# Kernel tuning notes

Measured on AMD Instinct MI355X. Metric: run time of the kernel, lower is better.

Reference implementation:

```python
import jax, jax.numpy as jnp
import numpy as np


def _segsum(x):
    """Stable segment sum: exp(segsum(A)) is 1-semiseparable. x: (..., T) -> (..., T, T)."""
    T = x.shape[-1]
    xx = jnp.broadcast_to(x[..., None], (*x.shape, T))
    xx = jnp.where(jnp.tril(jnp.ones((T, T), bool), -1), xx, 0.0)
    s = jnp.cumsum(xx, axis=-2)
    return jnp.where(jnp.tril(jnp.ones((T, T), bool), 0), s, -jnp.inf)


def setup_inputs() -> dict:
    key = jax.random.key(0)
    ks = jax.random.split(key, 6)
    b, T, h, p, n = 2, 1024, 32, 64, 128
    x = jax.random.normal(ks[0], (b, T, h, p), jnp.float32)
    # negative decay rates, as produced by -exp(A_log)*softplus(dt) in Mamba2
    A = -jax.random.uniform(ks[1], (b, T, h), jnp.float32, minval=0.01, maxval=0.5)
    B = jax.random.normal(ks[2], (b, T, h, n), jnp.float32)
    C = jax.random.normal(ks[3], (b, T, h, n), jnp.float32)
    # retrieval similarity mask (lower-triangular, like segment_and_cosine_similarity output)
    L_mask = jax.random.uniform(ks[4], (b, h, T, T), jnp.float32) * jnp.tril(jnp.ones((T, T), jnp.float32))
    mask_scaling_factor = jnp.float32(0.5)
    return {"x": x, "A": A, "B": B, "C": C, "L_mask": L_mask,
            "mask_scaling_factor": mask_scaling_factor, "chunk_size": 64}


def reference(x, A, B, C, L_mask, mask_scaling_factor, chunk_size):
    b, T, h, p = x.shape
    n = B.shape[-1]
    l = chunk_size
    k = T // l
    # chunk: b (c l) ... -> b c l ...
    xr = x.reshape(b, k, l, h, p)
    Br = B.reshape(b, k, l, h, n)
    Cr = C.reshape(b, k, l, h, n)
    Ar = jnp.transpose(A.reshape(b, k, l, h), (0, 3, 1, 2))  # b h c l
    A_cs = jnp.cumsum(Ar, axis=-1)                            # b h c l
    L = jnp.exp(_segsum(Ar))                                  # b h c l l
    # decompose_diagonal_and_lower_tri(L_mask, chunk_size)
    r = L_mask.reshape(b, h, k, l, k, l)
    didx = np.arange(k)
    L_mask_diag = jnp.moveaxis(r[:, :, didx, :, didx, :], 0, 2)          # b h k l l
    row_idx, col_idx = np.tril_indices(k, -1)                             # strict lower block pairs
    lower_tri = jnp.moveaxis(r[:, :, row_idx, :, col_idx, :], 0, 2)       # b h P l l
    L = L + mask_scaling_factor * L_mask_diag
    # diagonal (intra-chunk) blocks
    Y_diag = jnp.einsum('bclhn,bcshn,bhcls,bcshp->bclhp', Cr, Br, L, xr)
    # retrieval off-diagonal blocks, scatter-added back per destination chunk
    Y_tmp = jnp.einsum('bclhn,bcshn,bhcls,bcshp->bclhp',
                       Cr[:, row_idx], Br[:, col_idx],
                       mask_scaling_factor * lower_tri, xr[:, col_idx])   # b P l h p
    Y_retr = jnp.moveaxis(
        jax.ops.segment_sum(jnp.moveaxis(Y_tmp, 1, 0), jnp.asarray(row_idx), num_segments=k),
        0, 1)                                                             # b k l h p
    # inter-chunk state passing
    decay_states = jnp.exp(A_cs[..., -1:] - A_cs)                         # b h c l
    states = jnp.einsum('bclhn,bhcl,bclhp->bchpn', Br, decay_states, xr)  # b c h p n
    states = jnp.concatenate([jnp.zeros_like(states[:, :1]), states], axis=1)
    decay_chunk = jnp.exp(_segsum(jnp.pad(A_cs[..., -1], ((0, 0), (0, 0), (1, 0)))))  # b h (k+1) (k+1)
    new_states = jnp.einsum('bhzc,bchpn->bzhpn', decay_chunk, states)
    states_in, final_state = new_states[:, :-1], new_states[:, -1]
    Y_off = jnp.einsum('bclhn,bchpn,bhcl->bclhp', Cr, states_in, jnp.exp(A_cs))
    Y = (Y_diag + Y_off + Y_retr).reshape(b, T, h, p)
    return Y, final_state
```

## Files before the change

### kernel.cpp

```cpp
#include <hip/hip_runtime.h>

#define T_ 1024
#define H_ 32
#define P_ 64
#define N_ 128
#define L_ 64

typedef float f32x4 __attribute__((ext_vector_type(4)));
typedef short short8 __attribute__((ext_vector_type(8)));
typedef short short4v __attribute__((ext_vector_type(4)));

static __device__ __forceinline__ unsigned short f2bf(float f) {
  unsigned int u = __float_as_uint(f);
  u = u + 0x7fffu + ((u >> 16) & 1u);
  return (unsigned short)(u >> 16);
}

__global__ __launch_bounds__(1024) void cuma_kernel(const float* __restrict__ A,
                                                    float* __restrict__ cumA) {
  const int bh = blockIdx.x;
  const int b = bh >> 5, h = bh & 31;
  const int t = threadIdx.x;
  __shared__ float s[1024];
  s[t] = A[(b * T_ + t) * H_ + h];
  __syncthreads();
  for (int off = 1; off < 1024; off <<= 1) {
    float v = (t >= off) ? s[t - off] : 0.0f;
    __syncthreads();
    s[t] += v;
    __syncthreads();
  }
  cumA[bh * T_ + t] = s[t];
}

__global__ __launch_bounds__(256, 3) void attn_kernel(
    const float* __restrict__ x, const float* __restrict__ Bm,
    const float* __restrict__ Cm, const float* __restrict__ mask,
    const float* __restrict__ msf_p, const float* __restrict__ cumA,
    float* __restrict__ Y) {
  const int qc = 15 - (int)blockIdx.x;
  const int bh = blockIdx.y;
  const int b = bh >> 5, h = bh & 31;
  const float msf = msf_p[0];

  __shared__ short Cs[64][136];
  __shared__ short Bs[64][136];
  __shared__ short Xt[64][72];
  __shared__ short Ps[64][72];
  __shared__ float cAq[64];
  __shared__ float cAk[64];

  const int tid = threadIdx.x;
  const int wv = tid >> 6;
  const int lane = tid & 63;
  const int q = lane >> 4;
  const int c = lane & 15;

  {
    const float* Cg = Cm + ((size_t)(b * T_ + qc * L_) * H_ + h) * N_;
#pragma unroll
    for (int it = 0; it < 8; ++it) {
      const int idx = tid + 256 * it;
      const int row = idx >> 5, k4 = idx & 31;
      const float4 v = *(const float4*)(Cg + (size_t)row * (H_ * N_) + k4 * 4);
      short4v o;
      o.x = (short)f2bf(v.x); o.y = (short)f2bf(v.y);
      o.z = (short)f2bf(v.z); o.w = (short)f2bf(v.w);
      *(short4v*)&Cs[row][k4 * 4] = o;
    }
    if (tid < 64) cAq[tid] = cumA[bh * T_ + qc * L_ + tid];
  }

  f32x4 yacc[4];
#pragma unroll
  for (int pt = 0; pt < 4; ++pt) yacc[pt] = (f32x4){0.f, 0.f, 0.f, 0.f};

  for (int kc = 0; kc <= qc; ++kc) {
    float m_pre[16];
    {
      const float* mbase = mask + ((size_t)bh * T_ + (size_t)(qc * L_ + 16 * wv + 4 * q)) * T_ +
                           (size_t)kc * L_ + c;
#pragma unroll
      for (int tj = 0; tj < 4; ++tj)
#pragma unroll
        for (int r = 0; r < 4; ++r)
          m_pre[tj * 4 + r] = mbase[(size_t)r * T_ + 16 * tj];
    }

    __syncthreads();

    {
      const float* Bg = Bm + ((size_t)(b * T_ + kc * L_) * H_ + h) * N_;
#pragma unroll
      for (int it = 0; it < 8; ++it) {
        const int idx = tid + 256 * it;
        const int row = idx >> 5, k4 = idx & 31;
        const float4 v = *(const float4*)(Bg + (size_t)row * (H_ * N_) + k4 * 4);
        short4v o;
        o.x = (short)f2bf(v.x); o.y = (short)f2bf(v.y);
        o.z = (short)f2bf(v.z); o.w = (short)f2bf(v.w);
        *(short4v*)&Bs[row][k4 * 4] = o;
      }
      const float* xg = x + ((size_t)(b * T_ + kc * L_) * H_ + h) * P_;
#pragma unroll
      for (int it = 0; it < 4; ++it) {
        const int idx = tid + 256 * it;
        const int j = idx >> 4, p4 = idx & 15;
        const float4 v = *(const float4*)(xg + (size_t)j * (H_ * P_) + p4 * 4);
        Xt[p4 * 4 + 0][j] = (short)f2bf(v.x);
        Xt[p4 * 4 + 1][j] = (short)f2bf(v.y);
        Xt[p4 * 4 + 2][j] = (short)f2bf(v.z);
        Xt[p4 * 4 + 3][j] = (short)f2bf(v.w);
      }
      if (tid < 64) cAk[tid] = cumA[bh * T_ + kc * L_ + tid];
    }
    __syncthreads();

    f32x4 sacc[4];
#pragma unroll
    for (int tj = 0; tj < 4; ++tj) sacc[tj] = (f32x4){0.f, 0.f, 0.f, 0.f};
#pragma unroll
    for (int kt = 0; kt < 4; ++kt) {
      const int k0 = kt * 32;
      const short8 af = *(const short8*)&Cs[16 * wv + c][k0 + 8 * q];
#pragma unroll
      for (int tj = 0; tj < 4; ++tj) {
        const short8 bf = *(const short8*)&Bs[16 * tj + c][k0 + 8 * q];
        sacc[tj] = __builtin_amdgcn_mfma_f32_16x16x32_bf16(af, bf, sacc[tj], 0, 0, 0);
      }
    }

    float ca_i[4], ck_j[4];
#pragma unroll
    for (int r = 0; r < 4; ++r) ca_i[r] = cAq[16 * wv + 4 * q + r];
#pragma unroll
    for (int tj = 0; tj < 4; ++tj) ck_j[tj] = cAk[16 * tj + c];
    const bool diag = (kc == qc);
#pragma unroll
    for (int tj = 0; tj < 4; ++tj) {
      const int j_l = 16 * tj + c;
#pragma unroll
      for (int r = 0; r < 4; ++r) {
        const int i_l = 16 * wv + 4 * q + r;
        float wgt = __expf(ca_i[r] - ck_j[tj]) + msf * m_pre[tj * 4 + r];
        if (diag && j_l > i_l) wgt = 0.0f;
        Ps[i_l][j_l] = (short)f2bf(sacc[tj][r] * wgt);
      }
    }
    __syncthreads();

#pragma unroll
    for (int kt = 0; kt < 2; ++kt) {
      const int k0 = kt * 32;
      const short8 pf = *(const short8*)&Ps[16 * wv + c][k0 + 8 * q];
#pragma unroll
      for (int pt = 0; pt < 4; ++pt) {
        const short8 xf = *(const short8*)&Xt[16 * pt + c][k0 + 8 * q];
        yacc[pt] = __builtin_amdgcn_mfma_f32_16x16x32_bf16(pf, xf, yacc[pt], 0, 0, 0);
      }
    }
  }

  float* Yg = Y + ((size_t)(b * T_ + qc * L_) * H_ + h) * P_;
#pragma unroll
  for (int pt = 0; pt < 4; ++pt)
#pragma unroll
    for (int r = 0; r < 4; ++r)
      Yg[(size_t)(16 * wv + 4 * q + r) * (H_ * P_) + 16 * pt + c] = yacc[pt][r];
}

__global__ __launch_bounds__(512) void state_kernel(
    const float* __restrict__ x, const float* __restrict__ Bm,
    const float* __restrict__ cumA, float* __restrict__ out) {
  const int bh = blockIdx.x;
  const int pg = blockIdx.y;
  const int b = bh >> 5, h = bh & 31;
  const int tid = threadIdx.x;
  const int n = tid & 127;
  const int th = tid >> 7;
  const int pbase = pg * 8;

  __shared__ float wsh[1024];
  __shared__ float red[3][8][128];
  {
    const float cend = cumA[bh * T_ + (T_ - 1)];
    for (int t = tid; t < 1024; t += 512)
      wsh[t] = __expf(cend - cumA[bh * T_ + t]);
  }
  __syncthreads();

  float acc[8];
#pragma unroll
  for (int pp = 0; pp < 8; ++pp) acc[pp] = 0.0f;

  const int t0 = th * 256;
#pragma unroll 4
  for (int it = 0; it < 256; ++it) {
    const int t = t0 + it;
    const float bv = Bm[((size_t)(b * T_ + t) * H_ + h) * N_ + n] * wsh[t];
    const float* xp = x + ((size_t)(b * T_ + t) * H_ + h) * P_ + pbase;
#pragma unroll
    for (int pp = 0; pp < 8; ++pp) acc[pp] += bv * xp[pp];
  }

  if (th > 0) {
#pragma unroll
    for (int pp = 0; pp < 8; ++pp) red[th - 1][pp][n] = acc[pp];
  }
  __syncthreads();
  if (th == 0) {
    float* o = out + (size_t)bh * P_ * N_;
#pragma unroll
    for (int pp = 0; pp < 8; ++pp) {
      const float s = acc[pp] + red[0][pp][n] + red[1][pp][n] + red[2][pp][n];
      o[(size_t)(pbase + pp) * N_ + n] = s;
    }
  }
}

extern "C" void kernel_launch(void* const* d_in, const int* in_sizes, int n_in,
                              void* d_out, int out_size, void* d_ws, size_t ws_size,
                              hipStream_t stream) {
  const float* x    = (const float*)d_in[0];
  const float* A    = (const float*)d_in[1];
  const float* Bm   = (const float*)d_in[2];
  const float* Cm   = (const float*)d_in[3];
  const float* mask = (const float*)d_in[4];
  const float* msf  = (const float*)d_in[5];
  float* Y  = (float*)d_out;
  float* fs = (float*)d_out + (size_t)2 * T_ * H_ * P_;
  float* cumA = (float*)d_ws;

  cuma_kernel<<<64, 1024, 0, stream>>>(A, cumA);
  attn_kernel<<<dim3(16, 64), 256, 0, stream>>>(x, Bm, Cm, mask, msf, cumA, Y);
  state_kernel<<<dim3(64, 8), 512, 0, stream>>>(x, Bm, cumA, fs);
}
```

Before: 539.6 us.

## Pre-convert B and x to bf16 layouts and use MFMA for final state

Adds prep kernels that convert B and x to bf16 once, including transposed copies, stored in workspace. The attention kernel then reads those operands straight from global memory into MFMA fragments with no shared-memory staging or block barriers, keeps C fragments in registers, and orders blocks so that all heads of one query chunk are launched together. The state kernel is rewritten to use bf16 MFMA over the transposed tensors instead of scalar FP32 FMAs. This removes the repeated per-block conversion of B and x, but adds extra launches and workspace traffic, and the final state now uses bf16 rounding of the decay-weighted x.

Result: no change. 539.0 us (-0.1%).

```diff
diff --git a/kernel.cpp b/kernel.cpp
--- a/kernel.cpp
+++ b/kernel.cpp
@@ -12,8 +12,11 @@
 
 static __device__ __forceinline__ unsigned short f2bf(float f) {
   unsigned int u = __float_as_uint(f);
-  u = u + 0x7fffu + ((u >> 16) & 1u);
+  u += 0x7fffu + ((u >> 16) & 1u);
   return (unsigned short)(u >> 16);
+}
+static __device__ __forceinline__ float bf2f(short s) {
+  return __uint_as_float(((unsigned int)(unsigned short)s) << 16);
 }
 
 __global__ __launch_bounds__(1024) void cuma_kernel(const float* __restrict__ A,
@@ -33,155 +36,185 @@
   cumA[bh * T_ + t] = s[t];
 }
 
-__global__ __launch_bounds__(256, 3) void attn_kernel(
-    const float* __restrict__ x, const float* __restrict__ Bm,
+__global__ __launch_bounds__(256) void prep_b(const float* __restrict__ Bm,
+                                              short* __restrict__ Bbf,
+                                              short* __restrict__ BT) {
+  const int bh = blockIdx.x;
+  const int tb = blockIdx.y;
+  const int b = bh >> 5, h = bh & 31;
+  const int tid = threadIdx.x;
+  __shared__ short Bt[128][72];
+#pragma unroll
+  for (int i = 0; i < 8; ++i) {
+    const int idx = tid + 256 * i;
+    const int row = idx >> 5, n4 = idx & 31;
+    const float4 v = *(const float4*)(Bm + ((size_t)(b * T_ + tb * 64 + row) * H_ + h) * N_ + n4 * 4);
+    short4v o;
+    o.x = (short)f2bf(v.x); o.y = (short)f2bf(v.y);
+    o.z = (short)f2bf(v.z); o.w = (short)f2bf(v.w);
+    *(short4v*)(Bbf + ((size_t)bh * T_ + tb * 64 + row) * N_ + n4 * 4) = o;
+    Bt[n4 * 4 + 0][row] = o.x; Bt[n4 * 4 + 1][row] = o.y;
+    Bt[n4 * 4 + 2][row] = o.z; Bt[n4 * 4 + 3][row] = o.w;
+  }
+  __syncthreads();
+#pragma unroll
+  for (int i = 0; i < 4; ++i) {
+    const int idx = tid + 256 * i;
+    const int n = idx >> 3, t8 = idx & 7;
+    const short4v a = *(const short4v*)&Bt[n][t8 * 8];
+    const short4v c = *(const short4v*)&Bt[n][t8 * 8 + 4];
+    short8 o;
+    o[0] = a.x; o[1] = a.y; o[2] = a.z; o[3] = a.w;
+    o[4] = c.x; o[5] = c.y; o[6] = c.z; o[7] = c.w;
+    *(short8*)(BT + ((size_t)bh * N_ + n) * T_ + tb * 64 + t8 * 8) = o;
+  }
+}
+
+__global__ __launch_bounds__(256) void prep_x(const float* __restrict__ x,
+                                              short* __restrict__ xT) {
+  const int bh = blockIdx.x, tb = blockIdx.y;
+  const int b = bh >> 5, h = bh & 31;
+  const int tid = threadIdx.x;
+  __shared__ short Xt[64][72];
+#pragma unroll
+  for (int i = 0; i < 4; ++i) {
+    const int idx = tid + 256 * i;
+    const int row = idx >> 4, p4 = idx & 15;
+    const float4 v = *(const float4*)(x + ((size_t)(b * T_ + tb * 64 + row) * H_ + h) * P_ + p4 * 4);
+    Xt[p4 * 4 + 0][row] = (short)f2bf(v.x);
+    Xt[p4 * 4 + 1][row] = (short)f2bf(v.y);
+    Xt[p4 * 4 + 2][row] = (short)f2bf(v.z);
+    Xt[p4 * 4 + 3][row] = (short)f2bf(v.w);
+  }
+  __syncthreads();
+#pragma unroll
+  for (int i = 0; i < 2; ++i) {
+    const int idx = tid + 256 * i;
+    const int p = idx >> 3, t8 = idx & 7;
+    const short4v a = *(const short4v*)&Xt[p][t8 * 8];
+    const short4v c = *(const short4v*)&Xt[p][t8 * 8 + 4];
+    short8 o;
+    o[0] = a.x; o[1] = a.y; o[2] = a.z; o[3] = a.w;
+    o[4] = c.x; o[5] = c.y; o[6] = c.z; o[7] = c.w;
+    *(short8*)(xT + ((size_t)bh * P_ + p) * T_ + tb * 64 + t8 * 8) = o;
+  }
+}
+
+__global__ __launch_bounds__(256, 4) void attn_kernel(
+    const short* __restrict__ xT, const short* __restrict__ Bbf,
     const float* __restrict__ Cm, const float* __restrict__ mask,
     const float* __restrict__ msf_p, const float* __restrict__ cumA,
     float* __restrict__ Y) {
-  const int qc = 15 - (int)blockIdx.x;
-  const int bh = blockIdx.y;
+  const int blk = blockIdx.x;
+  const int qc = 15 - (blk >> 6);
+  const int bh = blk & 63;
   const int b = bh >> 5, h = bh & 31;
   const float msf = msf_p[0];
-
-  __shared__ short Cs[64][136];
-  __shared__ short Bs[64][136];
-  __shared__ short Xt[64][72];
-  __shared__ short Ps[64][72];
-  __shared__ float cAq[64];
-  __shared__ float cAk[64];
-
-  const int tid = threadIdx.x;
-  const int wv = tid >> 6;
+  const int tid = threadIdx.x;
+  const int w = tid >> 6;
   const int lane = tid & 63;
-  const int q = lane >> 4;
-  const int c = lane & 15;
-
+  const int q = lane >> 4, c = lane & 15;
+
+  __shared__ short Ps[4][16][72];
+
+  short8 cf[4];
   {
-    const float* Cg = Cm + ((size_t)(b * T_ + qc * L_) * H_ + h) * N_;
-#pragma unroll
-    for (int it = 0; it < 8; ++it) {
-      const int idx = tid + 256 * it;
-      const int row = idx >> 5, k4 = idx & 31;
-      const float4 v = *(const float4*)(Cg + (size_t)row * (H_ * N_) + k4 * 4);
-      short4v o;
-      o.x = (short)f2bf(v.x); o.y = (short)f2bf(v.y);
-      o.z = (short)f2bf(v.z); o.w = (short)f2bf(v.w);
-      *(short4v*)&Cs[row][k4 * 4] = o;
-    }
-    if (tid < 64) cAq[tid] = cumA[bh * T_ + qc * L_ + tid];
-  }
+    const float* Cg = Cm + ((size_t)(b * T_ + qc * L_ + 16 * w + c) * H_ + h) * N_ + 8 * q;
+#pragma unroll
+    for (int kt = 0; kt < 4; ++kt) {
+      const float4 v0 = *(const float4*)(Cg + kt * 32);
+      const float4 v1 = *(const float4*)(Cg + kt * 32 + 4);
+      short8 f;
+      f[0] = (short)f2bf(v0.x); f[1] = (short)f2bf(v0.y);
+      f[2] = (short)f2bf(v0.z); f[3] = (short)f2bf(v0.w);
+      f[4] = (short)f2bf(v1.x); f[5] = (short)f2bf(v1.y);
+      f[6] = (short)f2bf(v1.z); f[7] = (short)f2bf(v1.w);
+      cf[kt] = f;
+    }
+  }
+  float ca_i[4];
+#pragma unroll
+  for (int r = 0; r < 4; ++r)
+    ca_i[r] = cumA[bh * T_ + qc * L_ + 16 * w + 4 * q + r];
 
   f32x4 yacc[4];
 #pragma unroll
   for (int pt = 0; pt < 4; ++pt) yacc[pt] = (f32x4){0.f, 0.f, 0.f, 0.f};
 
   for (int kc = 0; kc <= qc; ++kc) {
-    float m_pre[16];
+    float mv[16];
     {
-      const float* mbase = mask + ((size_t)bh * T_ + (size_t)(qc * L_ + 16 * wv + 4 * q)) * T_ +
+      const float* mbase = mask + ((size_t)bh * T_ + (size_t)(qc * L_ + 16 * w + 4 * q)) * T_ +
                            (size_t)kc * L_ + c;
 #pragma unroll
       for (int tj = 0; tj < 4; ++tj)
 #pragma unroll
         for (int r = 0; r < 4; ++r)
-          m_pre[tj * 4 + r] = mbase[(size_t)r * T_ + 16 * tj];
-    }
-
-    __syncthreads();
-
-    {
-      const float* Bg = Bm + ((size_t)(b * T_ + kc * L_) * H_ + h) * N_;
-#pragma unroll
-      for (int it = 0; it < 8; ++it) {
-        const int idx = tid + 256 * it;
-        const int row = idx >> 5, k4 = idx & 31;
-        const float4 v = *(const float4*)(Bg + (size_t)row * (H_ * N_) + k4 * 4);
-        short4v o;
-        o.x = (short)f2bf(v.x); o.y = (short)f2bf(v.y);
-        o.z = (short)f2bf(v.z); o.w = (short)f2bf(v.w);
-        *(short4v*)&Bs[row][k4 * 4] = o;
+          mv[tj * 4 + r] = mbase[(size_t)r * T_ + 16 * tj];
+    }
+    float ck[4];
+#pragma unroll
+    for (int tj = 0; tj < 4; ++tj)
+      ck[tj] = cumA[bh * T_ + kc * L_ + 16 * tj + c];
+
+    f32x4 sacc[4];
+#pragma unroll
+    for (int tj = 0; tj < 4; ++tj) sacc[tj] = (f32x4){0.f, 0.f, 0.f, 0.f};
+    const short* Bg = Bbf + ((size_t)bh * T_ + kc * L_) * N_ + 8 * q;
+#pragma unroll
+    for (int kt = 0; kt < 4; ++kt) {
+#pragma unroll
+      for (int tj = 0; tj < 4; ++tj) {
+        const short8 bf = *(const short8*)(Bg + (size_t)(16 * tj + c) * N_ + kt * 32);
+        sacc[tj] = __builtin_amdgcn_mfma_f32_16x16x32_bf16(cf[kt], bf, sacc[tj], 0, 0, 0);
       }
-      const float* xg = x + ((size_t)(b * T_ + kc * L_) * H_ + h) * P_;
-#pragma unroll
-      for (int it = 0; it < 4; ++it) {
-        const int idx = tid + 256 * it;
-        const int j = idx >> 4, p4 = idx & 15;
-        const float4 v = *(const float4*)(xg + (size_t)j * (H_ * P_) + p4 * 4);
-        Xt[p4 * 4 + 0][j] = (short)f2bf(v.x);
-        Xt[p4 * 4 + 1][j] = (short)f2bf(v.y);
-        Xt[p4 * 4 + 2][j] = (short)f2bf(v.z);
-        Xt[p4 * 4 + 3][j] = (short)f2bf(v.w);
-      }
-      if (tid < 64) cAk[tid] = cumA[bh * T_ + kc * L_ + tid];
-    }
-    __syncthreads();
-
-    f32x4 sacc[4];
-#pragma unroll
-    for (int tj = 0; tj < 4; ++tj) sacc[tj] = (f32x4){0.f, 0.f, 0.f, 0.f};
-#pragma unroll
-    for (int kt = 0; kt < 4; ++kt) {
-      const int k0 = kt * 32;
-      const short8 af = *(const short8*)&Cs[16 * wv + c][k0 + 8 * q];
-#pragma unroll
-      for (int tj = 0; tj < 4; ++tj) {
-        const short8 bf = *(const short8*)&Bs[16 * tj + c][k0 + 8 * q];
-        sacc[tj] = __builtin_amdgcn_mfma_f32_16x16x32_bf16(af, bf, sacc[tj], 0, 0, 0);
-      }
-    }
-
-    float ca_i[4], ck_j[4];
-#pragma unroll
-    for (int r = 0; r < 4; ++r) ca_i[r] = cAq[16 * wv + 4 * q + r];
-#pragma unroll
-    for (int tj = 0; tj < 4; ++tj) ck_j[tj] = cAk[16 * tj + c];
+    }
+
     const bool diag = (kc == qc);
 #pragma unroll
     for (int tj = 0; tj < 4; ++tj) {
       const int j_l = 16 * tj + c;
 #pragma unroll
       for (int r = 0; r < 4; ++r) {
-        const int i_l = 16 * wv + 4 * q + r;
-        float wgt = __expf(ca_i[r] - ck_j[tj]) + msf * m_pre[tj * 4 + r];
+        const int i_l = 16 * w + 4 * q + r;
+        float wgt = __expf(ca_i[r] - ck[tj]) + msf * mv[tj * 4 + r];
         if (diag && j_l > i_l) wgt = 0.0f;
-        Ps[i_l][j_l] = (short)f2bf(sacc[tj][r] * wgt);
+        Ps[w][4 * q + r][j_l] = (short)f2bf(sacc[tj][r] * wgt);
       }
     }
-    __syncthreads();
-
-#pragma unroll
-    for (int kt = 0; kt < 2; ++kt) {
-      const int k0 = kt * 32;
-      const short8 pf = *(const short8*)&Ps[16 * wv + c][k0 + 8 * q];
+
+#pragma unroll
+    for (int kt2 = 0; kt2 < 2; ++kt2) {
+      const short8 pf = *(const short8*)&Ps[w][c][kt2 * 32 + 8 * q];
+      const short* xg = xT + (size_t)bh * P_ * T_ + kc * L_ + kt2 * 32 + 8 * q;
 #pragma unroll
       for (int pt = 0; pt < 4; ++pt) {
-        const short8 xf = *(const short8*)&Xt[16 * pt + c][k0 + 8 * q];
+        const short8 xf = *(const short8*)(xg + (size_t)(16 * pt + c) * T_);
         yacc[pt] = __builtin_amdgcn_mfma_f32_16x16x32_bf16(pf, xf, yacc[pt], 0, 0, 0);
       }
     }
   }
 
-  float* Yg = Y + ((size_t)(b * T_ + qc * L_) * H_ + h) * P_;
+  float* Yg = Y + ((size_t)(b * T_ + qc * L_ + 16 * w + 4 * q) * H_ + h) * P_;
 #pragma unroll
   for (int pt = 0; pt < 4; ++pt)
 #pragma unroll
     for (int r = 0; r < 4; ++r)
-      Yg[(size_t)(16 * wv + 4 * q + r) * (H_ * P_) + 16 * pt + c] = yacc[pt][r];
+      Yg[(size_t)r * (H_ * P_) + 16 * pt + c] = yacc[pt][r];
 }
 
 __global__ __launch_bounds__(512) void state_kernel(
-    const float* __restrict__ x, const float* __restrict__ Bm,
+    const short* __restrict__ xT, const short* __restrict__ BT,
     const float* __restrict__ cumA, float* __restrict__ out) {
   const int bh = blockIdx.x;
-  const int pg = blockIdx.y;
-  const int b = bh >> 5, h = bh & 31;
-  const int tid = threadIdx.x;
-  const int n = tid & 127;
-  const int th = tid >> 7;
-  const int pbase = pg * 8;
+  const int tid = threadIdx.x;
+  const int w = (tid >> 6) & 3;
+  const int th = tid >> 8;
+  const int lane = tid & 63;
+  const int q = lane >> 4, c = lane & 15;
 
   __shared__ float wsh[1024];
-  __shared__ float red[3][8][128];
+  __shared__ float red[4][16][128];
   {
     const float cend = cumA[bh * T_ + (T_ - 1)];
     for (int t = tid; t < 1024; t += 512)
@@ -189,32 +222,42 @@
   }
   __syncthreads();
 
-  float acc[8];
-#pragma unroll
-  for (int pp = 0; pp < 8; ++pp) acc[pp] = 0.0f;
-
-  const int t0 = th * 256;
-#pragma unroll 4
-  for (int it = 0; it < 256; ++it) {
-    const int t = t0 + it;
-    const float bv = Bm[((size_t)(b * T_ + t) * H_ + h) * N_ + n] * wsh[t];
-    const float* xp = x + ((size_t)(b * T_ + t) * H_ + h) * P_ + pbase;
-#pragma unroll
-    for (int pp = 0; pp < 8; ++pp) acc[pp] += bv * xp[pp];
-  }
-
-  if (th > 0) {
-#pragma unroll
-    for (int pp = 0; pp < 8; ++pp) red[th - 1][pp][n] = acc[pp];
+  f32x4 acc[8];
+#pragma unroll
+  for (int nt = 0; nt < 8; ++nt) acc[nt] = (f32x4){0.f, 0.f, 0.f, 0.f};
+
+  for (int ktl = 0; ktl < 16; ++ktl) {
+    const int t0 = th * 512 + ktl * 32;
+    const short8 xv = *(const short8*)(xT + ((size_t)bh * P_ + 16 * w + c) * T_ + t0 + 8 * q);
+    const float4 w0 = *(const float4*)&wsh[t0 + 8 * q];
+    const float4 w1 = *(const float4*)&wsh[t0 + 8 * q + 4];
+    short8 af;
+    af[0] = (short)f2bf(bf2f(xv[0]) * w0.x); af[1] = (short)f2bf(bf2f(xv[1]) * w0.y);
+    af[2] = (short)f2bf(bf2f(xv[2]) * w0.z); af[3] = (short)f2bf(bf2f(xv[3]) * w0.w);
+    af[4] = (short)f2bf(bf2f(xv[4]) * w1.x); af[5] = (short)f2bf(bf2f(xv[5]) * w1.y);
+    af[6] = (short)f2bf(bf2f(xv[6]) * w1.z); af[7] = (short)f2bf(bf2f(xv[7]) * w1.w);
+#pragma unroll
+    for (int nt = 0; nt < 8; ++nt) {
+      const short8 bf = *(const short8*)(BT + ((size_t)bh * N_ + 16 * nt + c) * T_ + t0 + 8 * q);
+      acc[nt] = __builtin_amdgcn_mfma_f32_16x16x32_bf16(af, bf, acc[nt], 0, 0, 0);
+    }
+  }
+
+  if (th == 1) {
+#pragma unroll
+    for (int nt = 0; nt < 8; ++nt)
+#pragma unroll
+      for (int r = 0; r < 4; ++r) red[w][4 * q + r][16 * nt + c] = acc[nt][r];
   }
   __syncthreads();
   if (th == 0) {
     float* o = out + (size_t)bh * P_ * N_;
 #pragma unroll
-    for (int pp = 0; pp < 8; ++pp) {
-      const float s = acc[pp] + red[0][pp][n] + red[1][pp][n] + red[2][pp][n];
-      o[(size_t)(pbase + pp) * N_ + n] = s;
-    }
+    for (int nt = 0; nt < 8; ++nt)
+#pragma unroll
+      for (int r = 0; r < 4; ++r)
+        o[(size_t)(16 * w + 4 * q + r) * N_ + 16 * nt + c] =
+            acc[nt][r] + red[w][4 * q + r][16 * nt + c];
   }
 }
 
@@ -229,9 +272,16 @@
   const float* msf  = (const float*)d_in[5];
   float* Y  = (float*)d_out;
   float* fs = (float*)d_out + (size_t)2 * T_ * H_ * P_;
-  float* cumA = (float*)d_ws;
+
+  char* ws = (char*)d_ws;
+  float* cumA = (float*)ws;
+  short* Bbf  = (short*)(ws + (1 << 18));
+  short* BT   = (short*)(ws + (1 << 18) + (size_t)64 * T_ * N_ * 2);
+  short* xT   = (short*)(ws + (1 << 18) + (size_t)128 * T_ * N_ * 2);
 
   cuma_kernel<<<64, 1024, 0, stream>>>(A, cumA);
-  attn_kernel<<<dim3(16, 64), 256, 0, stream>>>(x, Bm, Cm, mask, msf, cumA, Y);
-  state_kernel<<<dim3(64, 8), 512, 0, stream>>>(x, Bm, cumA, fs);
-}
+  prep_b<<<dim3(64, 16), 256, 0, stream>>>(Bm, Bbf, BT);
+  prep_x<<<dim3(64, 16), 256, 0, stream>>>(x, xT);
+  attn_kernel<<<1024, 256, 0, stream>>>(xT, Bbf, Cm, mask, msf, cumA, Y);
+  state_kernel<<<64, 512, 0, stream>>>(xT, BT, cumA, fs);
+}
```
